# Performance work log

Measured on AMD Instinct MI355X. Metric: run time of the kernel, lower is better.

The kernel has to match this reference:

```python
import jax, jax.numpy as jnp
import numpy as np

B, T, DKQ, DV, EKQ, EV, H, OUT = 8, 2048, 64, 64, 128, 128, 4, 32
FF = 4 * EV
NEG = -1e30  # additive mask value (safe stand-in for -inf)


def _ln(x, g, b, eps=1e-5):
    m = x.mean(-1, keepdims=True)
    var = ((x - m) ** 2).mean(-1, keepdims=True)
    return (x - m) * jax.lax.rsqrt(var + eps) * g + b


def _attn(q, k, v, mask):
    # q,k,v: [n, T, E] -> heads [n, H, T, dh]; NOTE: no 1/sqrt(d) scaling (faithful to source)
    n, t, _ = q.shape
    q = q.reshape(n, t, H, -1).transpose(0, 2, 1, 3)
    k = k.reshape(n, t, H, -1).transpose(0, 2, 1, 3)
    v = v.reshape(n, t, H, -1).transpose(0, 2, 1, 3)
    w = jnp.einsum('bhqd,bhkd->bhqk', q, k) + mask  # [n,H,T,T]
    a = jax.nn.softmax(w, axis=-1)
    o = jnp.einsum('bhqk,bhkd->bhqd', a, v)
    return o.transpose(0, 2, 1, 3).reshape(n, t, -1)


def setup_inputs() -> dict:
    key = jax.random.key(0)
    ks = jax.random.split(key, 32)
    w = lambda k, s: jax.random.normal(k, s, jnp.float32) * 0.02
    DIN_A = DKQ + DV
    return {
        'kq': jax.random.normal(ks[0], (B, T, DKQ), jnp.float32),
        'v': jax.random.normal(ks[1], (B, T, DV), jnp.float32),
        # Layer A (input_dim = DKQ+DV, embed = EV)
        'A_Wk': w(ks[2], (DIN_A, EV)), 'A_bk': jnp.zeros((EV,), jnp.float32),
        'A_Wq': w(ks[3], (DIN_A, EV)), 'A_bq': jnp.zeros((EV,), jnp.float32),
        'A_Wv': w(ks[4], (DIN_A, EV)), 'A_bv': jnp.zeros((EV,), jnp.float32),
        'A_f1W': w(ks[5], (EV, FF)), 'A_f1b': jnp.zeros((FF,), jnp.float32),
        'A_f2W': w(ks[6], (FF, EV)), 'A_f2b': jnp.zeros((EV,), jnp.float32),
        'A_n1g': jnp.ones((EV,), jnp.float32), 'A_n1b': jnp.zeros((EV,), jnp.float32),
        'A_n2g': jnp.ones((EV,), jnp.float32), 'A_n2b': jnp.zeros((EV,), jnp.float32),
        # Layer B (kq -> EKQ, vA -> EV)
        'B_Wk': w(ks[7], (DKQ, EKQ)), 'B_bk': jnp.zeros((EKQ,), jnp.float32),
        'B_Wq': w(ks[8], (DKQ, EKQ)), 'B_bq': jnp.zeros((EKQ,), jnp.float32),
        'B_Wv': w(ks[9], (EV, EV)), 'B_bv': jnp.zeros((EV,), jnp.float32),
        'B_f1W': w(ks[10], (EV, FF)), 'B_f1b': jnp.zeros((FF,), jnp.float32),
        'B_f2W': w(ks[11], (FF, EV)), 'B_f2b': jnp.zeros((EV,), jnp.float32),
        # Output head
        'out_W': w(ks[12], (EV, OUT)), 'out_b': jnp.zeros((OUT,), jnp.float32),
    }


def reference(kq, v, A_Wk, A_bk, A_Wq, A_bq, A_Wv, A_bv, A_f1W, A_f1b, A_f2W, A_f2b,
              A_n1g, A_n1b, A_n2g, A_n2b, B_Wk, B_bk, B_Wq, B_bq, B_Wv, B_bv,
              B_f1W, B_f1b, B_f2W, B_f2b, out_W, out_b):
    n, t, _ = kq.shape
    i = jnp.arange(t)[:, None]
    j = jnp.arange(t)[None, :]
    mask_a = jnp.where(j <= i, 0.0, NEG).astype(jnp.float32)               # causal (diag=1)
    mask_b = jnp.where((j < i) | ((i == 0) & (j == 0)), 0.0, NEG).astype(jnp.float32)  # strict causal + (0,0) exception

    # ---- Layer A ----
    X = jnp.concatenate([kq, v], axis=-1)
    K = X @ A_Wk + A_bk
    Q = X @ A_Wq + A_bq
    V = X @ A_Wv + A_bv
    attn_out = _attn(Q, K, V, mask_a)
    h1 = _ln(V + attn_out, A_n1g, A_n1b)
    ff = jax.nn.gelu(h1 @ A_f1W + A_f1b, approximate=False) @ A_f2W + A_f2b
    vA = _ln(h1 + ff, A_n2g, A_n2b)

    # ---- Layer B (no residuals / norms: values is overwritten in source) ----
    K2 = kq @ B_Wk + B_bk
    Q2 = kq @ B_Wq + B_bq
    V2 = vA @ B_Wv + B_bv
    attn_out2 = _attn(Q2, K2, V2, mask_b)
    ff2 = jax.nn.gelu(attn_out2 @ B_f1W + B_f1b, approximate=False) @ B_f2W + B_f2b

    return ff2 @ out_W + out_b
```

## Files before the change

kernel.cpp:

```cpp
#include <hip/hip_runtime.h>
#include <hip/hip_bf16.h>

#define TSEQ 2048
#define NBATCH 8
#define NROWS (NBATCH*TSEQ)
#define EMB 128
#define NH 4
#define DH 32
#define OUTD 32
#define APLANE (NROWS*EMB)
#define LOG2E 1.44269504088896340736f

typedef short s8v __attribute__((ext_vector_type(8)));
typedef short s4v __attribute__((ext_vector_type(4)));
typedef float f4v __attribute__((ext_vector_type(4)));

__device__ __forceinline__ unsigned short f2bf(float f){
  unsigned int u = __float_as_uint(f);
  unsigned int r = u + 0x7fffu + ((u >> 16) & 1u);
  return (unsigned short)(r >> 16);
}
__device__ __forceinline__ float bf2f(unsigned short u){
  return __uint_as_float(((unsigned int)u) << 16);
}
__device__ __forceinline__ float exp2fast(float x){
#if __has_builtin(__builtin_amdgcn_exp2f)
  return __builtin_amdgcn_exp2f(x);
#else
  return __expf(x * 0.6931471805599453f);
#endif
}

struct WPack {
  const float* src[10];
  int off[10];
  int ntk[10];
  int rowoff[10];
  int nsh[10];
  int kn[10];
};
__global__ __launch_bounds__(256) void prep(WPack p, short* __restrict__ warena,
                                            const float* __restrict__ kq, const float* __restrict__ v,
                                            unsigned short* __restrict__ X){
  int blk = blockIdx.x;
  if (blk < (NROWS*EMB/256)){
    int idx = blk*256 + threadIdx.x;
    int row = idx >> 7, c = idx & 127;
    float val = (c < 64) ? kq[row*64 + c] : v[row*64 + (c-64)];
    unsigned short hi = f2bf(val);
    X[idx]          = hi;
    X[idx + APLANE] = f2bf(val - bf2f(hi));
    return;
  }
  blk -= (NROWS*EMB/256);
  int m = 0;
  #pragma unroll
  for (int i=0;i<10;i++){
    int nb = p.kn[i] >> 8;
    if (blk < nb){ m = i; break; }
    blk -= nb;
  }
  int idx = blk*256 + threadIdx.x;
  float x = p.src[m][idx];
  int nsh = p.nsh[m];
  int n = idx & ((1<<nsh)-1);
  int k = idx >> nsh;
  int K = p.kn[m] >> nsh;
  unsigned short hi = f2bf(x);
  unsigned short lo = f2bf(x - bf2f(hi));
  short* dh = warena + p.off[m] + (size_t)(p.rowoff[m] + n)*K + k;
  dh[0]        = (short)hi;
  dh[p.ntk[m]] = (short)lo;
}

struct GOuts {
  const float* bias[3];
  float* of[3];
  unsigned short* ob[3];
  float scl[3];
};
template<int CT>
__global__ __launch_bounds__(256) void gemm2(
    const unsigned short* __restrict__ A, int aplane, int lda, int K, int niter,
    const short* __restrict__ wt, int NTK,
    GOuts og, int NT, int nseg, int act,
    unsigned short* __restrict__ vtb, int vcol0){
  __shared__ short As[2][2][64*40];
  const int tid  = threadIdx.x;
  const int w    = tid >> 6;
  const int lane = tid & 63;
  const int col  = lane & 15;
  const int quad = lane >> 4;
  const int row0 = blockIdx.x * 64;
  const int cb   = blockIdx.y*(64*CT) + w*(16*CT) + col;
  const bool two = (aplane != 0);

  f4v acc[4][CT];
  #pragma unroll
  for (int i=0;i<4;i++)
    #pragma unroll
    for (int j=0;j<CT;j++) acc[i][j] = (f4v){0.f,0.f,0.f,0.f};

  const int ar = tid >> 2, ac = (tid & 3)*8;
  const unsigned short* abase = A + (size_t)(row0 + ar)*lda;

  s8v pah, pal;
  pah = *(const s8v*)(abase + ac);
  if (two) pal = *(const s8v*)(abase + aplane + ac);

  const short* wbase[CT];
  #pragma unroll
  for (int ct=0;ct<CT;ct++) wbase[ct] = wt + (size_t)(cb + ct*16)*K + quad*8;

  for (int i=0;i<niter;i++){
    const int buf = i & 1;
    *(s8v*)&As[buf][0][ar*40 + ac] = pah;
    if (two) *(s8v*)&As[buf][1][ar*40 + ac] = pal;
    __syncthreads();
    if (i+1 < niter){
      const int kcol = (i+1)*32 + ac;
      pah = *(const s8v*)(abase + kcol);
      if (two) pal = *(const s8v*)(abase + aplane + kcol);
    }
    s8v bh[CT], bl[CT];
    #pragma unroll
    for (int ct=0;ct<CT;ct++){
      bh[ct] = *(const s8v*)(wbase[ct] + i*32);
      bl[ct] = *(const s8v*)(wbase[ct] + i*32 + NTK);
    }
    #pragma unroll
    for (int rt=0;rt<4;rt++){
      s8v ah = *(const s8v*)&As[buf][0][(rt*16 + col)*40 + quad*8];
      #pragma unroll
      for (int ct=0;ct<CT;ct++)
        acc[rt][ct] = __builtin_amdgcn_mfma_f32_16x16x32_bf16(ah, bh[ct], acc[rt][ct], 0, 0, 0);
      if (two){
        s8v al = *(const s8v*)&As[buf][1][(rt*16 + col)*40 + quad*8];
        #pragma unroll
        for (int ct=0;ct<CT;ct++)
          acc[rt][ct] = __builtin_amdgcn_mfma_f32_16x16x32_bf16(al, bh[ct], acc[rt][ct], 0, 0, 0);
      }
      #pragma unroll
      for (int ct=0;ct<CT;ct++)
        acc[rt][ct] = __builtin_amdgcn_mfma_f32_16x16x32_bf16(ah, bl[ct], acc[rt][ct], 0, 0, 0);
    }
  }

  const int NB = 64*CT;
  const int cb0 = (int)blockIdx.y * NB;
  const bool dotr = (vtb != nullptr) && (cb0 >= vcol0) && (cb0 < vcol0 + 128);
  short* Lt = &As[0][0][0];
  if (dotr) __syncthreads();

  #pragma unroll
  for (int ct=0;ct<CT;ct++){
    const int cg = cb + ct*16;
    int seg, lcol, ldc;
    if (nseg > 1){ seg = cg >> 7; lcol = cg & 127; ldc = 128; }
    else         { seg = 0; lcol = cg; ldc = NT; }
    const float bv = og.bias[seg][lcol];
    const float sc = og.scl[seg];
    float* of = og.of[seg];
    unsigned short* ob = og.ob[seg];
    #pragma unroll
    for (int rt=0;rt<4;rt++){
      s4v pk;
      #pragma unroll
      for (int r=0;r<4;r++){
        const int row = row0 + rt*16 + quad*4 + r;
        float val = acc[rt][ct][r] + bv;
        if (act == 1) val = 0.5f*val*(1.f + erff(val*0.70710678118654752440f));
        val *= sc;
        if (ob)      ob[(size_t)row*ldc + lcol] = f2bf(val);
        else if (of) of[(size_t)row*ldc + lcol] = val;
        if (dotr) pk[r] = (short)f2bf(val);
      }
      if (dotr)
        *(s4v*)&Lt[(w*(16*CT) + ct*16 + col)*72 + rt*16 + quad*4] = pk;
    }
  }
  if (dotr){
    __syncthreads();
    const int b = row0 >> 11, t0 = row0 & 2047;
    #pragma unroll
    for (int it=0; it<2*CT; it++){
      const int cl = it*32 + (tid>>3);
      const int t8 = (tid&7)*8;
      s8v o = *(const s8v*)&Lt[cl*72 + t8];
      const int cr = cb0 + cl - vcol0;
      *(s8v*)(vtb + ((size_t)((b*4 + (cr>>5))*32 + (cr&31)))*2048 + t0 + t8) = o;
    }
  }
}

#define KT_STRIDE 40
#define VT_STRIDE 72
#define PW_STRIDE 72
__global__ __launch_bounds__(256) void flash4(const unsigned short* __restrict__ Qb,
                                              const unsigned short* __restrict__ Kb,
                                              const unsigned short* __restrict__ Vtb,
                                              float* __restrict__ O0, float* __restrict__ O1,
                                              float* __restrict__ L0, float* __restrict__ L1,
                                              int mode){
  __shared__ short Kt[64*KT_STRIDE];
  __shared__ short Vt[32*VT_STRIDE];
  __shared__ short Pw[4][16*PW_STRIDE];
  const int tid  = threadIdx.x;
  const int w    = tid >> 6;
  const int lane = tid & 63;
  const int col  = lane & 15;
  const int quad = lane >> 4;
  const int bh = blockIdx.y;
  const int b = bh >> 2, h = bh & 3;
  const int par = blockIdx.z;
  float* Op = par ? O1 : O0;
  float* Lp = par ? L1 : L0;
  const int qt = (int)((blockIdx.x + blockIdx.y) & 31);
  const int qbase = qt*64 + w*16;
  const int jtmax = qt;

  const int kr = tid >> 2, kc8 = (tid & 3)*8;
  const int vd = tid >> 3, vk8 = (tid & 7)*8;

  s8v qf = *(const s8v*)(Qb + (size_t)(b*TSEQ + qbase + col)*EMB + h*DH + quad*8);
  f4v o0 = {0.f,0.f,0.f,0.f}, o1 = {0.f,0.f,0.f,0.f};
  float lr[4] = {0.f,0.f,0.f,0.f};

  if (par <= jtmax){
    s8v ka, va;
    ka = *(const s8v*)(Kb + (size_t)(b*TSEQ + par*64 + kr)*EMB + h*DH + kc8);
    va = *(const s8v*)(Vtb + ((size_t)bh*32 + vd)*TSEQ + par*64 + vk8);
    for (int jt = par; jt <= jtmax; jt += 2){
      __syncthreads();
      *(s8v*)&Kt[kr*KT_STRIDE + kc8] = ka;
      *(s8v*)&Vt[vd*VT_STRIDE + vk8] = va;
      __syncthreads();
      if (jt + 2 <= jtmax){
        ka = *(const s8v*)(Kb + (size_t)(b*TSEQ + (jt+2)*64 + kr)*EMB + h*DH + kc8);
        va = *(const s8v*)(Vtb + ((size_t)bh*32 + vd)*TSEQ + (jt+2)*64 + vk8);
      }
      f4v s[4];
      #pragma unroll
      for (int t4=0;t4<4;t4++){
        s8v kf = *(const s8v*)&Kt[(t4*16 + col)*KT_STRIDE + quad*8];
        f4v z = {0.f,0.f,0.f,0.f};
        s[t4] = __builtin_amdgcn_mfma_f32_16x16x32_bf16(qf, kf, z, 0, 0, 0);
      }
      if (jt == jtmax){
        const int j0 = jt*64;
        #pragma unroll
        for (int t4=0;t4<4;t4++){
          const int jg = j0 + t4*16 + col;
          #pragma unroll
          for (int r=0;r<4;r++){
            const int qg = qbase + quad*4 + r;
            const bool ok = (mode==0) ? (jg <= qg) : ((jg < qg) || (qg==0 && jg==0));
            s[t4][r] = ok ? s[t4][r] : -1e30f;
          }
        }
      }
      #pragma unroll
      for (int t4=0;t4<4;t4++){
        #pragma unroll
        for (int r=0;r<4;r++){
          float pv = exp2fast(s[t4][r]);
          s[t4][r] = pv;
          lr[r] += pv;
          Pw[w][(quad*4+r)*PW_STRIDE + t4*16 + col] = (short)f2bf(pv);
        }
      }
      #pragma unroll
      for (int kk=0;kk<2;kk++){
        s8v pf  = *(const s8v*)&Pw[w][col*PW_STRIDE + kk*32 + quad*8];
        s8v vf0 = *(const s8v*)&Vt[(col)*VT_STRIDE    + kk*32 + quad*8];
        s8v vf1 = *(const s8v*)&Vt[(16+col)*VT_STRIDE + kk*32 + quad*8];
        o0 = __builtin_amdgcn_mfma_f32_16x16x32_bf16(pf, vf0, o0, 0, 0, 0);
        o1 = __builtin_amdgcn_mfma_f32_16x16x32_bf16(pf, vf1, o1, 0, 0, 0);
      }
    }
  }
  float* obase = Op + (size_t)(b*TSEQ + qbase)*EMB + h*DH;
  #pragma unroll
  for (int r=0;r<4;r++){
    float l = lr[r];
    l += __shfl_xor(l,1); l += __shfl_xor(l,2);
    l += __shfl_xor(l,4); l += __shfl_xor(l,8);
    obase[(size_t)(quad*4+r)*EMB + col]      = o0[r];
    obase[(size_t)(quad*4+r)*EMB + 16 + col] = o1[r];
    if (col == 0) Lp[(size_t)(b*TSEQ + qbase + quad*4 + r)*NH + h] = l;
  }
}

__global__ __launch_bounds__(256) void combine_ln(const float* __restrict__ O0, const float* __restrict__ O1,
                                                  const float* __restrict__ L0, const float* __restrict__ L1,
                                                  const float* __restrict__ Vf,
                                                  const float* __restrict__ g, const float* __restrict__ bt,
                                                  unsigned short* __restrict__ outp){
  const int row = blockIdx.x*4 + (threadIdx.x >> 6);
  const int tid = threadIdx.x & 63;
  const size_t base = (size_t)row*EMB;
  const int h0 = tid >> 5, h1i = 2 + (tid >> 5);
  const float la = L0[(size_t)row*NH + h0] + L1[(size_t)row*NH + h0];
  const float lb = L0[(size_t)row*NH + h1i] + L1[(size_t)row*NH + h1i];
  float x0 = Vf[base+tid]    + (O0[base+tid]    + O1[base+tid])    / la;
  float x1 = Vf[base+tid+64] + (O0[base+tid+64] + O1[base+tid+64]) / lb;
  float s  = x0 + x1;
  float s2 = x0*x0 + x1*x1;
  #pragma unroll
  for (int off=1; off<64; off<<=1){
    s  += __shfl_xor(s,  off);
    s2 += __shfl_xor(s2, off);
  }
  float mean = s * (1.f/128.f);
  float var  = s2 * (1.f/128.f) - mean*mean;
  float rstd = rsqrtf(var + 1e-5f);
  float y0 = (x0-mean)*rstd*g[tid]    + bt[tid];
  float y1 = (x1-mean)*rstd*g[tid+64] + bt[tid+64];
  unsigned short h0b = f2bf(y0), h1b = f2bf(y1);
  outp[base+tid]             = h0b;
  outp[base+tid+64]          = h1b;
  outp[base+tid+APLANE]      = f2bf(y0 - bf2f(h0b));
  outp[base+tid+64+APLANE]   = f2bf(y1 - bf2f(h1b));
}

__global__ __launch_bounds__(256) void ln2(const unsigned short* __restrict__ Xp, const float* __restrict__ R,
                                           const float* __restrict__ g, const float* __restrict__ bt,
                                           unsigned short* __restrict__ outp){
  const int row = blockIdx.x*4 + (threadIdx.x >> 6);
  const int tid = threadIdx.x & 63;
  const size_t base = (size_t)row*EMB;
  float x0 = bf2f(Xp[base+tid])    + bf2f(Xp[base+tid+APLANE])    + R[base+tid];
  float x1 = bf2f(Xp[base+tid+64]) + bf2f(Xp[base+tid+64+APLANE]) + R[base+tid+64];
  float s  = x0 + x1;
  float s2 = x0*x0 + x1*x1;
  #pragma unroll
  for (int off=1; off<64; off<<=1){
    s  += __shfl_xor(s,  off);
    s2 += __shfl_xor(s2, off);
  }
  float mean = s * (1.f/128.f);
  float var  = s2 * (1.f/128.f) - mean*mean;
  float rstd = rsqrtf(var + 1e-5f);
  float y0 = (x0-mean)*rstd*g[tid]    + bt[tid];
  float y1 = (x1-mean)*rstd*g[tid+64] + bt[tid+64];
  unsigned short h0b = f2bf(y0), h1b = f2bf(y1);
  outp[base+tid]             = h0b;
  outp[base+tid+64]          = h1b;
  outp[base+tid+APLANE]      = f2bf(y0 - bf2f(h0b));
  outp[base+tid+64+APLANE]   = f2bf(y1 - bf2f(h1b));
}

__global__ __launch_bounds__(256) void combine_b(const float* __restrict__ O0, const float* __restrict__ O1,
                                                 const float* __restrict__ L0, const float* __restrict__ L1,
                                                 unsigned short* __restrict__ outp){
  const int idx = blockIdx.x*256 + threadIdx.x;
  const int row = idx >> 7, c = idx & 127, h = c >> 5;
  const float l = L0[(size_t)row*NH + h] + L1[(size_t)row*NH + h];
  const float v = (O0[idx] + O1[idx]) / l;
  unsigned short hb = f2bf(v);
  outp[idx]          = hb;
  outp[idx + APLANE] = f2bf(v - bf2f(hb));
}

__global__ __launch_bounds__(256) void out_proj(const float* __restrict__ A,
                                                const float* __restrict__ W, const float* __restrict__ bb,
                                                float* __restrict__ out){
  __shared__ float As[8*128];
  __shared__ float Ws2[128*32];
  const int tid = threadIdx.x;
  const int row0 = blockIdx.x * 8;
  for (int idx = tid; idx < 8*128; idx += 256) As[idx] = A[(size_t)row0*128 + idx];
  for (int idx = tid; idx < 128*32; idx += 256) Ws2[idx] = W[idx];
  __syncthreads();
  const int r = tid >> 5, c = tid & 31;
  float acc = bb[c];
  #pragma unroll 8
  for (int k=0;k<128;k++) acc = fmaf(As[r*128 + k], Ws2[k*32 + c], acc);
  out[(size_t)(row0 + r)*OUTD + c] = acc;
}

extern "C" void kernel_launch(void* const* d_in, const int* in_sizes, int n_in,
                              void* d_out, int out_size, void* d_ws, size_t ws_size,
                              hipStream_t stream) {
  const float* kq    = (const float*)d_in[0];
  const float* v     = (const float*)d_in[1];
  const float* A_Wk  = (const float*)d_in[2];  const float* A_bk  = (const float*)d_in[3];
  const float* A_Wq  = (const float*)d_in[4];  const float* A_bq  = (const float*)d_in[5];
  const float* A_Wv  = (const float*)d_in[6];  const float* A_bv  = (const float*)d_in[7];
  const float* A_f1W = (const float*)d_in[8];  const float* A_f1b = (const float*)d_in[9];
  const float* A_f2W = (const float*)d_in[10]; const float* A_f2b = (const float*)d_in[11];
  const float* A_n1g = (const float*)d_in[12]; const float* A_n1b = (const float*)d_in[13];
  const float* A_n2g = (const float*)d_in[14]; const float* A_n2b = (const float*)d_in[15];
  const float* B_Wk  = (const float*)d_in[16]; const float* B_bk  = (const float*)d_in[17];
  const float* B_Wq  = (const float*)d_in[18]; const float* B_bq  = (const float*)d_in[19];
  const float* B_Wv  = (const float*)d_in[20]; const float* B_bv  = (const float*)d_in[21];
  const float* B_f1W = (const float*)d_in[22]; const float* B_f1b = (const float*)d_in[23];
  const float* B_f2W = (const float*)d_in[24]; const float* B_f2b = (const float*)d_in[25];
  const float* out_W = (const float*)d_in[26]; const float* out_b = (const float*)d_in[27];
  float* out = (float*)d_out;
  (void)in_sizes; (void)n_in; (void)out_size; (void)ws_size;

  char* ws = (char*)d_ws;
  const size_t MB = 1024*1024;
  short* warena = (short*)ws;
  unsigned short* Xs  = (unsigned short*)(ws + 2*MB);
  unsigned short* Qbf = (unsigned short*)(ws + 10*MB);
  unsigned short* Kbf = (unsigned short*)(ws + 14*MB);
  unsigned short* Vtb = (unsigned short*)(ws + 18*MB);
  float* Vf  = (float*)(ws + 22*MB);
  float* O0  = (float*)(ws + 30*MB);
  float* O1  = (float*)(ws + 38*MB);
  float* L0  = (float*)(ws + 46*MB);
  float* L1  = (float*)(ws + 47*MB);
  unsigned short* h1p = (unsigned short*)(ws + 48*MB);
  unsigned short* mid = (unsigned short*)(ws + 56*MB);
  float* ffo = (float*)(ws + 72*MB);
  unsigned short* vAp = (unsigned short*)(ws + 80*MB);

  WPack p;
  const float* srcs[10] = {A_Wq,A_Wk,A_Wv,A_f1W,A_f2W,B_Wq,B_Wk,B_Wv,B_f1W,B_f2W};
  int kn[10]     = {16384,16384,16384,65536,65536,8192,8192,16384,65536,65536};
  int nsh[10]    = {7,7,7,9,7,7,7,7,9,7};
  int off[10]    = {0,0,0,98304,229376,360448,360448,393216,425984,557056};
  int ntk[10]    = {49152,49152,49152,65536,65536,16384,16384,16384,65536,65536};
  int rowoff[10] = {0,128,256,0,0,0,128,0,0,0};
  int nblk = 0;
  for (int i=0;i<10;i++){
    p.src[i]=srcs[i]; p.kn[i]=kn[i]; p.nsh[i]=nsh[i];
    p.off[i]=off[i]; p.ntk[i]=ntk[i]; p.rowoff[i]=rowoff[i];
    nblk += kn[i] >> 8;
  }
  prep<<<(NROWS*EMB/256) + nblk, 256, 0, stream>>>(p, warena, kq, v, Xs);

  GOuts oQKVA = {{A_bq,A_bk,A_bv},{nullptr,nullptr,Vf},{Qbf,Kbf,nullptr},{LOG2E,1.f,1.f}};
  GOuts oF1A  = {{A_f1b,nullptr,nullptr},{nullptr,nullptr,nullptr},{mid,nullptr,nullptr},{1.f,1.f,1.f}};
  GOuts oF2A  = {{A_f2b,nullptr,nullptr},{ffo,nullptr,nullptr},{nullptr,nullptr,nullptr},{1.f,1.f,1.f}};
  GOuts oQKB  = {{B_bq,B_bk,nullptr},{nullptr,nullptr,nullptr},{Qbf,Kbf,nullptr},{LOG2E,1.f,1.f}};
  GOuts oVB   = {{B_bv,nullptr,nullptr},{nullptr,nullptr,nullptr},{nullptr,nullptr,nullptr},{1.f,1.f,1.f}};
  GOuts oF1B  = {{B_f1b,nullptr,nullptr},{nullptr,nullptr,nullptr},{mid,nullptr,nullptr},{1.f,1.f,1.f}};
  GOuts oF2B  = {{B_f2b,nullptr,nullptr},{ffo,nullptr,nullptr},{nullptr,nullptr,nullptr},{1.f,1.f,1.f}};

  gemm2<2><<<dim3(256,3), 256, 0, stream>>>(Xs, APLANE, 128, 128, 4, warena + 0,      49152, oQKVA, 384, 3, 0, Vtb, 256);
  flash4<<<dim3(32,32,2), 256, 0, stream>>>(Qbf, Kbf, Vtb, O0, O1, L0, L1, 0);
  combine_ln<<<NROWS/4, 256, 0, stream>>>(O0, O1, L0, L1, Vf, A_n1g, A_n1b, h1p);
  gemm2<2><<<dim3(256,4), 256, 0, stream>>>(h1p, APLANE, 128, 128, 4, warena + 98304, 65536, oF1A, 512, 1, 1, nullptr, 0);
  gemm2<1><<<dim3(256,2), 256, 0, stream>>>(mid, 0,      512, 512, 16, warena + 229376, 65536, oF2A, 128, 1, 0, nullptr, 0);
  ln2<<<NROWS/4, 256, 0, stream>>>(h1p, ffo, A_n2g, A_n2b, vAp);

  gemm2<2><<<dim3(256,2), 256, 0, stream>>>(Xs, APLANE, 128, 64, 2,  warena + 360448, 16384, oQKB, 256, 2, 0, nullptr, 0);
  gemm2<1><<<dim3(256,2), 256, 0, stream>>>(vAp, APLANE, 128, 128, 4, warena + 393216, 16384, oVB, 128, 1, 0, Vtb, 0);
  flash4<<<dim3(32,32,2), 256, 0, stream>>>(Qbf, Kbf, Vtb, O0, O1, L0, L1, 1);
  combine_b<<<NROWS*128/256, 256, 0, stream>>>(O0, O1, L0, L1, h1p);
  gemm2<2><<<dim3(256,4), 256, 0, stream>>>(h1p, APLANE, 128, 128, 4, warena + 425984, 65536, oF1B, 512, 1, 1, nullptr, 0);
  gemm2<1><<<dim3(256,2), 256, 0, stream>>>(mid, 0,      512, 512, 16, warena + 557056, 65536, oF2B, 128, 1, 0, nullptr, 0);

  out_proj<<<NROWS/8, 256, 0, stream>>>(ffo, out_W, out_b, out);
}
```

Measured before the change: 317.1 us.

## Rewrite causal attention with 32x32 MFMA, 128-row query tiles and 4-way key split

Replaces the flash kernel with a version where each wave handles 32 query rows using 32x32x16 bf16 MFMAs. S is computed as K·Q so the P tile stays in registers and moves across lanes by shuffle, with no LDS round trip. Each block processes two paired query tiles (15-x and x) to balance causal work, and keys are split four ways instead of two. LDS tiles get an XOR swizzle to reduce bank conflicts, and packed bf16 conversion uses an inline instruction. In exchange, the combine kernels must read and sum four partial O/L planes, which roughly doubles the partial-output memory traffic and workspace use.

Measured after the change: 305.3 us. 3.7% less time.

```diff
diff --git a/kernel.cpp b/kernel.cpp
--- a/kernel.cpp
+++ b/kernel.cpp
@@ -10,10 +10,13 @@
 #define OUTD 32
 #define APLANE (NROWS*EMB)
 #define LOG2E 1.44269504088896340736f
+#define NPAR 4
 
 typedef short s8v __attribute__((ext_vector_type(8)));
 typedef short s4v __attribute__((ext_vector_type(4)));
 typedef float f4v __attribute__((ext_vector_type(4)));
+typedef float f16v __attribute__((ext_vector_type(16)));
+typedef unsigned int u4v __attribute__((ext_vector_type(4)));
 
 __device__ __forceinline__ unsigned short f2bf(float f){
   unsigned int u = __float_as_uint(f);
@@ -193,106 +196,113 @@
   }
 }
 
-#define KT_STRIDE 40
-#define VT_STRIDE 72
-#define PW_STRIDE 72
-__global__ __launch_bounds__(256) void flash4(const unsigned short* __restrict__ Qb,
-                                              const unsigned short* __restrict__ Kb,
-                                              const unsigned short* __restrict__ Vtb,
-                                              float* __restrict__ O0, float* __restrict__ O1,
-                                              float* __restrict__ L0, float* __restrict__ L1,
-                                              int mode){
-  __shared__ short Kt[64*KT_STRIDE];
-  __shared__ short Vt[32*VT_STRIDE];
-  __shared__ short Pw[4][16*PW_STRIDE];
+#define KSTR 40
+#define VSTR 72
+__device__ __forceinline__ int kswz(int row, int c){ return (row*KSTR + c) ^ (((row>>3)&3)<<3); }
+__device__ __forceinline__ int vswz(int row, int c){ return (row*VSTR + c) ^ (((row>>3)&3)<<3); }
+
+__global__ __launch_bounds__(256, 4) void flash5(const unsigned short* __restrict__ Qb,
+                                                 const unsigned short* __restrict__ Kb,
+                                                 const unsigned short* __restrict__ Vtb,
+                                                 float* __restrict__ O, float* __restrict__ L,
+                                                 int mode){
+  __shared__ short Kt[64*KSTR];
+  __shared__ short Vt[32*VSTR];
   const int tid  = threadIdx.x;
   const int w    = tid >> 6;
   const int lane = tid & 63;
-  const int col  = lane & 15;
-  const int quad = lane >> 4;
+  const int q31  = lane & 31;
+  const int hi   = lane >> 5;
   const int bh = blockIdx.y;
   const int b = bh >> 2, h = bh & 3;
   const int par = blockIdx.z;
-  float* Op = par ? O1 : O0;
-  float* Lp = par ? L1 : L0;
-  const int qt = (int)((blockIdx.x + blockIdx.y) & 31);
-  const int qbase = qt*64 + w*16;
-  const int jtmax = qt;
-
+  float* Op = O + (size_t)par*NROWS*EMB;
+  float* Lp = L + (size_t)par*NROWS*NH;
   const int kr = tid >> 2, kc8 = (tid & 3)*8;
   const int vd = tid >> 3, vk8 = (tid & 7)*8;
 
-  s8v qf = *(const s8v*)(Qb + (size_t)(b*TSEQ + qbase + col)*EMB + h*DH + quad*8);
-  f4v o0 = {0.f,0.f,0.f,0.f}, o1 = {0.f,0.f,0.f,0.f};
-  float lr[4] = {0.f,0.f,0.f,0.f};
-
-  if (par <= jtmax){
-    s8v ka, va;
-    ka = *(const s8v*)(Kb + (size_t)(b*TSEQ + par*64 + kr)*EMB + h*DH + kc8);
-    va = *(const s8v*)(Vtb + ((size_t)bh*32 + vd)*TSEQ + par*64 + vk8);
-    for (int jt = par; jt <= jtmax; jt += 2){
-      __syncthreads();
-      *(s8v*)&Kt[kr*KT_STRIDE + kc8] = ka;
-      *(s8v*)&Vt[vd*VT_STRIDE + vk8] = va;
-      __syncthreads();
-      if (jt + 2 <= jtmax){
-        ka = *(const s8v*)(Kb + (size_t)(b*TSEQ + (jt+2)*64 + kr)*EMB + h*DH + kc8);
-        va = *(const s8v*)(Vtb + ((size_t)bh*32 + vd)*TSEQ + (jt+2)*64 + vk8);
-      }
-      f4v s[4];
-      #pragma unroll
-      for (int t4=0;t4<4;t4++){
-        s8v kf = *(const s8v*)&Kt[(t4*16 + col)*KT_STRIDE + quad*8];
-        f4v z = {0.f,0.f,0.f,0.f};
-        s[t4] = __builtin_amdgcn_mfma_f32_16x16x32_bf16(qf, kf, z, 0, 0, 0);
-      }
-      if (jt == jtmax){
-        const int j0 = jt*64;
+  for (int pass = 0; pass < 2; pass++){
+    const int qt = pass ? (int)blockIdx.x : (15 - (int)blockIdx.x);
+    const int qbase = qt*128;
+    const int qrow  = qbase + w*32 + q31;
+    const int jtmax = 2*qt + 1;
+
+    s8v qB0 = *(const s8v*)(Qb + (size_t)(b*TSEQ + qrow)*EMB + h*DH + hi*8);
+    s8v qB1 = *(const s8v*)(Qb + (size_t)(b*TSEQ + qrow)*EMB + h*DH + 16 + hi*8);
+    f16v o;
+    #pragma unroll
+    for (int r=0;r<16;r++) o[r] = 0.f;
+    float lr = 0.f;
+
+    if (par <= jtmax){
+      s8v ka = *(const s8v*)(Kb + (size_t)(b*TSEQ + par*64 + kr)*EMB + h*DH + kc8);
+      s8v va = *(const s8v*)(Vtb + ((size_t)bh*32 + vd)*TSEQ + par*64 + vk8);
+      for (int jt = par; jt <= jtmax; jt += NPAR){
+        __syncthreads();
+        *(s8v*)&Kt[kswz(kr, kc8)] = ka;
+        *(s8v*)&Vt[vswz(vd, vk8)] = va;
+        __syncthreads();
+        if (jt + NPAR <= jtmax){
+          ka = *(const s8v*)(Kb + (size_t)(b*TSEQ + (jt+NPAR)*64 + kr)*EMB + h*DH + kc8);
+          va = *(const s8v*)(Vtb + ((size_t)bh*32 + vd)*TSEQ + (jt+NPAR)*64 + vk8);
+        }
+        const bool domask = (jt >= 2*qt);
         #pragma unroll
-        for (int t4=0;t4<4;t4++){
-          const int jg = j0 + t4*16 + col;
+        for (int kt=0;kt<2;kt++){
+          f16v s;
           #pragma unroll
-          for (int r=0;r<4;r++){
-            const int qg = qbase + quad*4 + r;
-            const bool ok = (mode==0) ? (jg <= qg) : ((jg < qg) || (qg==0 && jg==0));
-            s[t4][r] = ok ? s[t4][r] : -1e30f;
+          for (int r=0;r<16;r++) s[r] = 0.f;
+          {
+            s8v kf0 = *(const s8v*)&Kt[kswz(kt*32 + q31, hi*8)];
+            s = __builtin_amdgcn_mfma_f32_32x32x16_bf16(kf0, qB0, s, 0, 0, 0);
+            s8v kf1 = *(const s8v*)&Kt[kswz(kt*32 + q31, 16 + hi*8)];
+            s = __builtin_amdgcn_mfma_f32_32x32x16_bf16(kf1, qB1, s, 0, 0, 0);
+          }
+          if (domask){
+            #pragma unroll
+            for (int r=0;r<16;r++){
+              const int jg = jt*64 + kt*32 + (r&3) + 8*(r>>2) + 4*hi;
+              const bool ok = (mode==0) ? (jg <= qrow) : ((jg < qrow) || (qrow==0 && jg==0));
+              s[r] = ok ? s[r] : -1e30f;
+            }
+          }
+          #pragma unroll
+          for (int r=0;r<16;r++){ float pv = exp2fast(s[r]); s[r] = pv; lr += pv; }
+          unsigned P2[4][2];
+          #pragma unroll
+          for (int m=0;m<4;m++){
+            asm("v_cvt_pk_bf16_f32 %0, %1, %2" : "=v"(P2[m][0]) : "v"(s[4*m+0]), "v"(s[4*m+1]));
+            asm("v_cvt_pk_bf16_f32 %0, %1, %2" : "=v"(P2[m][1]) : "v"(s[4*m+2]), "v"(s[4*m+3]));
+          }
+          #pragma unroll
+          for (int kcl=0;kcl<2;kcl++){
+            const unsigned own0 = hi ? P2[2*kcl+1][0] : P2[2*kcl][0];
+            const unsigned own1 = hi ? P2[2*kcl+1][1] : P2[2*kcl][1];
+            const unsigned inv0 = hi ? P2[2*kcl][0]   : P2[2*kcl+1][0];
+            const unsigned inv1 = hi ? P2[2*kcl][1]   : P2[2*kcl+1][1];
+            const unsigned sx0 = (unsigned)__shfl_xor((int)inv0, 32);
+            const unsigned sx1 = (unsigned)__shfl_xor((int)inv1, 32);
+            u4v au;
+            au[0] = hi ? sx0 : own0;  au[1] = hi ? sx1 : own1;
+            au[2] = hi ? own0 : sx0;  au[3] = hi ? own1 : sx1;
+            s8v af = __builtin_bit_cast(s8v, au);
+            s8v vf = *(const s8v*)&Vt[vswz(q31, kt*32 + kcl*16 + hi*8)];
+            o = __builtin_amdgcn_mfma_f32_32x32x16_bf16(af, vf, o, 0, 0, 0);
           }
         }
       }
-      #pragma unroll
-      for (int t4=0;t4<4;t4++){
-        #pragma unroll
-        for (int r=0;r<4;r++){
-          float pv = exp2fast(s[t4][r]);
-          s[t4][r] = pv;
-          lr[r] += pv;
-          Pw[w][(quad*4+r)*PW_STRIDE + t4*16 + col] = (short)f2bf(pv);
-        }
-      }
-      #pragma unroll
-      for (int kk=0;kk<2;kk++){
-        s8v pf  = *(const s8v*)&Pw[w][col*PW_STRIDE + kk*32 + quad*8];
-        s8v vf0 = *(const s8v*)&Vt[(col)*VT_STRIDE    + kk*32 + quad*8];
-        s8v vf1 = *(const s8v*)&Vt[(16+col)*VT_STRIDE + kk*32 + quad*8];
-        o0 = __builtin_amdgcn_mfma_f32_16x16x32_bf16(pf, vf0, o0, 0, 0, 0);
-        o1 = __builtin_amdgcn_mfma_f32_16x16x32_bf16(pf, vf1, o1, 0, 0, 0);
-      }
-    }
-  }
-  float* obase = Op + (size_t)(b*TSEQ + qbase)*EMB + h*DH;
-  #pragma unroll
-  for (int r=0;r<4;r++){
-    float l = lr[r];
-    l += __shfl_xor(l,1); l += __shfl_xor(l,2);
-    l += __shfl_xor(l,4); l += __shfl_xor(l,8);
-    obase[(size_t)(quad*4+r)*EMB + col]      = o0[r];
-    obase[(size_t)(quad*4+r)*EMB + 16 + col] = o1[r];
-    if (col == 0) Lp[(size_t)(b*TSEQ + qbase + quad*4 + r)*NH + h] = l;
-  }
-}
-
-__global__ __launch_bounds__(256) void combine_ln(const float* __restrict__ O0, const float* __restrict__ O1,
-                                                  const float* __restrict__ L0, const float* __restrict__ L1,
+    }
+    const float lt = lr + __shfl_xor(lr, 32);
+    #pragma unroll
+    for (int r=0;r<16;r++){
+      const int ql = (r&3) + 8*(r>>2) + 4*hi;
+      Op[(size_t)(b*TSEQ + qbase + w*32 + ql)*EMB + h*DH + q31] = o[r];
+    }
+    if (hi == 0) Lp[(size_t)(b*TSEQ + qrow)*NH + h] = lt;
+  }
+}
+
+__global__ __launch_bounds__(256) void combine_ln(const float* __restrict__ O, const float* __restrict__ L,
                                                   const float* __restrict__ Vf,
                                                   const float* __restrict__ g, const float* __restrict__ bt,
                                                   unsigned short* __restrict__ outp){
@@ -300,10 +310,16 @@
   const int tid = threadIdx.x & 63;
   const size_t base = (size_t)row*EMB;
   const int h0 = tid >> 5, h1i = 2 + (tid >> 5);
-  const float la = L0[(size_t)row*NH + h0] + L1[(size_t)row*NH + h0];
-  const float lb = L0[(size_t)row*NH + h1i] + L1[(size_t)row*NH + h1i];
-  float x0 = Vf[base+tid]    + (O0[base+tid]    + O1[base+tid])    / la;
-  float x1 = Vf[base+tid+64] + (O0[base+tid+64] + O1[base+tid+64]) / lb;
+  float la = 0.f, lb = 0.f, s0 = 0.f, s1 = 0.f;
+  #pragma unroll
+  for (int p=0;p<NPAR;p++){
+    la += L[(size_t)p*NROWS*NH + (size_t)row*NH + h0];
+    lb += L[(size_t)p*NROWS*NH + (size_t)row*NH + h1i];
+    s0 += O[(size_t)p*NROWS*EMB + base + tid];
+    s1 += O[(size_t)p*NROWS*EMB + base + tid + 64];
+  }
+  float x0 = Vf[base+tid]    + s0/la;
+  float x1 = Vf[base+tid+64] + s1/lb;
   float s  = x0 + x1;
   float s2 = x0*x0 + x1*x1;
   #pragma unroll
@@ -350,13 +366,17 @@
   outp[base+tid+64+APLANE]   = f2bf(y1 - bf2f(h1b));
 }
 
-__global__ __launch_bounds__(256) void combine_b(const float* __restrict__ O0, const float* __restrict__ O1,
-                                                 const float* __restrict__ L0, const float* __restrict__ L1,
+__global__ __launch_bounds__(256) void combine_b(const float* __restrict__ O, const float* __restrict__ L,
                                                  unsigned short* __restrict__ outp){
   const int idx = blockIdx.x*256 + threadIdx.x;
   const int row = idx >> 7, c = idx & 127, h = c >> 5;
-  const float l = L0[(size_t)row*NH + h] + L1[(size_t)row*NH + h];
-  const float v = (O0[idx] + O1[idx]) / l;
+  float l = 0.f, ov = 0.f;
+  #pragma unroll
+  for (int p=0;p<NPAR;p++){
+    l  += L[(size_t)p*NROWS*NH + (size_t)row*NH + h];
+    ov += O[(size_t)p*NROWS*EMB + idx];
+  }
+  const float v = ov / l;
   unsigned short hb = f2bf(v);
   outp[idx]          = hb;
   outp[idx + APLANE] = f2bf(v - bf2f(hb));
@@ -408,14 +428,12 @@
   unsigned short* Kbf = (unsigned short*)(ws + 14*MB);
   unsigned short* Vtb = (unsigned short*)(ws + 18*MB);
   float* Vf  = (float*)(ws + 22*MB);
-  float* O0  = (float*)(ws + 30*MB);
-  float* O1  = (float*)(ws + 38*MB);
-  float* L0  = (float*)(ws + 46*MB);
-  float* L1  = (float*)(ws + 47*MB);
-  unsigned short* h1p = (unsigned short*)(ws + 48*MB);
-  unsigned short* mid = (unsigned short*)(ws + 56*MB);
-  float* ffo = (float*)(ws + 72*MB);
-  unsigned short* vAp = (unsigned short*)(ws + 80*MB);
+  float* Opar = (float*)(ws + 30*MB);
+  float* Lpar = (float*)(ws + 62*MB);
+  unsigned short* h1p = (unsigned short*)(ws + 66*MB);
+  unsigned short* mid = (unsigned short*)(ws + 74*MB);
+  float* ffo = (float*)(ws + 90*MB);
+  unsigned short* vAp = (unsigned short*)(ws + 98*MB);
 
   WPack p;
   const float* srcs[10] = {A_Wq,A_Wk,A_Wv,A_f1W,A_f2W,B_Wq,B_Wk,B_Wv,B_f1W,B_f2W};
@@ -441,16 +459,16 @@
   GOuts oF2B  = {{B_f2b,nullptr,nullptr},{ffo,nullptr,nullptr},{nullptr,nullptr,nullptr},{1.f,1.f,1.f}};
 
   gemm2<2><<<dim3(256,3), 256, 0, stream>>>(Xs, APLANE, 128, 128, 4, warena + 0,      49152, oQKVA, 384, 3, 0, Vtb, 256);
-  flash4<<<dim3(32,32,2), 256, 0, stream>>>(Qbf, Kbf, Vtb, O0, O1, L0, L1, 0);
-  combine_ln<<<NROWS/4, 256, 0, stream>>>(O0, O1, L0, L1, Vf, A_n1g, A_n1b, h1p);
+  flash5<<<dim3(8,32,NPAR), 256, 0, stream>>>(Qbf, Kbf, Vtb, Opar, Lpar, 0);
+  combine_ln<<<NROWS/4, 256, 0, stream>>>(Opar, Lpar, Vf, A_n1g, A_n1b, h1p);
   gemm2<2><<<dim3(256,4), 256, 0, stream>>>(h1p, APLANE, 128, 128, 4, warena + 98304, 65536, oF1A, 512, 1, 1, nullptr, 0);
   gemm2<1><<<dim3(256,2), 256, 0, stream>>>(mid, 0,      512, 512, 16, warena + 229376, 65536, oF2A, 128, 1, 0, nullptr, 0);
   ln2<<<NROWS/4, 256, 0, stream>>>(h1p, ffo, A_n2g, A_n2b, vAp);
 
   gemm2<2><<<dim3(256,2), 256, 0, stream>>>(Xs, APLANE, 128, 64, 2,  warena + 360448, 16384, oQKB, 256, 2, 0, nullptr, 0);
   gemm2<1><<<dim3(256,2), 256, 0, stream>>>(vAp, APLANE, 128, 128, 4, warena + 393216, 16384, oVB, 128, 1, 0, Vtb, 0);
-  flash4<<<dim3(32,32,2), 256, 0, stream>>>(Qbf, Kbf, Vtb, O0, O1, L0, L1, 1);
-  combine_b<<<NROWS*128/256, 256, 0, stream>>>(O0, O1, L0, L1, h1p);
+  flash5<<<dim3(8,32,NPAR), 256, 0, stream>>>(Qbf, Kbf, Vtb, Opar, Lpar, 1);
+  combine_b<<<NROWS*128/256, 256, 0, stream>>>(Opar, Lpar, h1p);
   gemm2<2><<<dim3(256,4), 256, 0, stream>>>(h1p, APLANE, 128, 128, 4, warena + 425984, 65536, oF1B, 512, 1, 1, nullptr, 0);
   gemm2<1><<<dim3(256,2), 256, 0, stream>>>(mid, 0,      512, 512, 16, warena + 557056, 65536, oF2B, 128, 1, 0, nullptr, 0);
 
```
